# Kernel tuning notes

Hardware: AMD Instinct MI355X
Metric: run time of the kernel (lower is better)

Reference implementation:

```python
import jax, jax.numpy as jnp
import numpy as np

B, T, D = 8, 4096, 1024


def setup_inputs() -> dict:
    key = jax.random.key(0)
    k1, k2 = jax.random.split(key)
    x = jax.random.normal(k1, (B, T, D), dtype=jnp.float32)
    lengths = jax.random.randint(k2, (B,), 0, T, dtype=jnp.int64)
    return {"x": x, "lengths": lengths}


def reference(x, lengths):
    # x: [B, T, D]; lengths: [B]
    # Original torch code materializes a [B,T,T,D] tensor via
    # (tril * pairwise_padding_mask)[..., None] * gelu(x)[:, None] and sums over
    # the source axis. Algebraically:
    #   out[b,i] = x[b,i] + m[b,i] * sum_{j<=i} m[b,j] * gelu(x[b,j])
    # where m[b,t] = (t < lengths[b]). This is a masked causal prefix sum.
    t = x.shape[1]
    valid = (jnp.arange(t)[None, :] < lengths[:, None]).astype(x.dtype)  # [B,T]
    g = jax.nn.gelu(x, approximate=False) * valid[:, :, None]           # [B,T,D]
    prefix = jnp.cumsum(g, axis=1)                                      # [B,T,D]
    return x + valid[:, :, None] * prefix
```

## Files before the change

### kernel.cpp

```cpp
#include <hip/hip_runtime.h>
#include <math.h>

#define BB 8
#define TT 4096
#define DD 1024
#define NC 64
#define CT (TT / NC)
#define D4 (DD / 4)

__device__ __forceinline__ float gelu_exact(float v) {
    return 0.5f * v * (1.0f + erff(v * 0.70710678118654752f));
}

__global__ __launch_bounds__(256)
void k_partial(const float* __restrict__ x, const int* __restrict__ lengths,
               float* __restrict__ ws) {
    const int c  = blockIdx.x;
    const int b  = blockIdx.y;
    const int d4 = threadIdx.x;
    const int len = lengths[b];
    const int t0 = c * CT;
    const int t1 = min(t0 + CT, len);

    const float4* __restrict__ xp = (const float4*)(x + (size_t)b * TT * DD);
    float4 s = make_float4(0.f, 0.f, 0.f, 0.f);
    #pragma unroll 4
    for (int t = t0; t < t1; ++t) {
        float4 v = xp[(size_t)t * D4 + d4];
        s.x += gelu_exact(v.x);
        s.y += gelu_exact(v.y);
        s.z += gelu_exact(v.z);
        s.w += gelu_exact(v.w);
    }
    ((float4*)ws)[((size_t)b * NC + c) * D4 + d4] = s;
}

__global__ __launch_bounds__(256)
void k_scan(float* __restrict__ ws) {
    const int b = blockIdx.y;
    const int d = blockIdx.x * 256 + threadIdx.x;
    float* p = ws + (size_t)b * NC * DD + d;
    float run = 0.f;
    #pragma unroll 8
    for (int c = 0; c < NC; ++c) {
        float v = p[(size_t)c * DD];
        p[(size_t)c * DD] = run;
        run += v;
    }
}

__global__ __launch_bounds__(256)
void k_apply(const float* __restrict__ x, const int* __restrict__ lengths,
             const float* __restrict__ ws, float* __restrict__ out) {
    const int c  = blockIdx.x;
    const int b  = blockIdx.y;
    const int d4 = threadIdx.x;
    const int len = lengths[b];
    const int t0 = c * CT;
    const int tv = min(t0 + CT, len);

    const float4* __restrict__ xp = (const float4*)(x + (size_t)b * TT * DD);
    float4* __restrict__ op = (float4*)(out + (size_t)b * TT * DD);

    float4 pre = ((const float4*)ws)[((size_t)b * NC + c) * D4 + d4];

    int t = t0;
    #pragma unroll 4
    for (; t < tv; ++t) {
        float4 v = xp[(size_t)t * D4 + d4];
        pre.x += gelu_exact(v.x);
        pre.y += gelu_exact(v.y);
        pre.z += gelu_exact(v.z);
        pre.w += gelu_exact(v.w);
        float4 o;
        o.x = v.x + pre.x;
        o.y = v.y + pre.y;
        o.z = v.z + pre.z;
        o.w = v.w + pre.w;
        op[(size_t)t * D4 + d4] = o;
    }
    #pragma unroll 4
    for (; t < t0 + CT; ++t) {
        op[(size_t)t * D4 + d4] = xp[(size_t)t * D4 + d4];
    }
}

extern "C" void kernel_launch(void* const* d_in, const int* in_sizes, int n_in,
                              void* d_out, int out_size, void* d_ws, size_t ws_size,
                              hipStream_t stream) {
    const float* x       = (const float*)d_in[0];
    const int*   lengths = (const int*)d_in[1];
    float*       out     = (float*)d_out;
    float*       ws      = (float*)d_ws;

    dim3 blk(256, 1, 1);
    dim3 g1(NC, BB, 1);
    hipLaunchKernelGGL(k_partial, g1, blk, 0, stream, x, lengths, ws);

    dim3 g2(DD / 256, BB, 1);
    hipLaunchKernelGGL(k_scan, g2, blk, 0, stream, ws);

    hipLaunchKernelGGL(k_apply, g1, blk, 0, stream, x, lengths, ws, out);
}
```

Measured before the change: 300.4 us.

## Raise chunk count and parallelize chunk scan with wave shuffles

Increases the number of time chunks from 64 to 256 so the partial and apply kernels launch 2048 blocks instead of 512, giving more occupancy across the GPU. The sequential per-column scan is replaced by a wave-level scan: each 64-lane wave handles one (batch, feature) column, with each lane holding 4 chunks and using shfl_up for the cross-lane prefix. The cost is more workspace traffic and scan memory accesses that are strided across columns and so not coalesced.

```diff
diff --git a/kernel.cpp b/kernel.cpp
--- a/kernel.cpp
+++ b/kernel.cpp
@@ -4,9 +4,10 @@
 #define BB 8
 #define TT 4096
 #define DD 1024
-#define NC 64
+#define NC 256
 #define CT (TT / NC)
 #define D4 (DD / 4)
+#define CPL (NC / 64)
 
 __device__ __forceinline__ float gelu_exact(float v) {
     return 0.5f * v * (1.0f + erff(v * 0.70710678118654752f));
@@ -37,16 +38,34 @@
 
 __global__ __launch_bounds__(256)
 void k_scan(float* __restrict__ ws) {
-    const int b = blockIdx.y;
-    const int d = blockIdx.x * 256 + threadIdx.x;
+    const int wave = threadIdx.x >> 6;
+    const int lane = threadIdx.x & 63;
+    const int col  = blockIdx.x * 4 + wave;
+    const int b = col >> 10;
+    const int d = col & (DD - 1);
+
     float* p = ws + (size_t)b * NC * DD + d;
-    float run = 0.f;
-    #pragma unroll 8
-    for (int c = 0; c < NC; ++c) {
-        float v = p[(size_t)c * DD];
-        p[(size_t)c * DD] = run;
-        run += v;
+    const int c0 = lane * CPL;
+
+    float v[CPL];
+    #pragma unroll
+    for (int k = 0; k < CPL; ++k) v[k] = p[(size_t)(c0 + k) * DD];
+
+    float tot = 0.f;
+    float loc[CPL];
+    #pragma unroll
+    for (int k = 0; k < CPL; ++k) { loc[k] = tot; tot += v[k]; }
+
+    float inc = tot;
+    #pragma unroll
+    for (int off = 1; off < 64; off <<= 1) {
+        float n = __shfl_up(inc, off, 64);
+        if (lane >= off) inc += n;
     }
+    const float excl = inc - tot;
+
+    #pragma unroll
+    for (int k = 0; k < CPL; ++k) p[(size_t)(c0 + k) * DD] = excl + loc[k];
 }
 
 __global__ __launch_bounds__(256)
@@ -97,7 +116,7 @@
     dim3 g1(NC, BB, 1);
     hipLaunchKernelGGL(k_partial, g1, blk, 0, stream, x, lengths, ws);
 
-    dim3 g2(DD / 256, BB, 1);
+    dim3 g2(BB * DD / 4, 1, 1);
     hipLaunchKernelGGL(k_scan, g2, blk, 0, stream, ws);
 
     hipLaunchKernelGGL(k_apply, g1, blk, 0, stream, x, lengths, ws, out);
```

Result: faster. 287.0 us (-4.4%).
